# Kernel tuning notes

Measured on AMD Instinct MI355X. Metric: run time of the kernel, lower is better.

Reference implementation:

```python
import jax, jax.numpy as jnp
import numpy as np


def setup_inputs() -> dict:
    key = jax.random.key(0)
    k1, k2, k3 = jax.random.split(key, 3)
    B, N, C_IN, C_OUT = 8, 2048, 128, 64
    x = jax.random.normal(k1, (B, N, C_IN), dtype=jnp.float32)
    # Linear(c_in, c_out): weight [c_out, c_in], bias [c_out]
    W_adj = jax.random.normal(k2, (C_OUT, C_IN), dtype=jnp.float32) * (1.0 / np.sqrt(C_IN))
    b_adj = jax.random.normal(k3, (C_OUT,), dtype=jnp.float32) * 0.01
    return {"x": x, "W_adj": W_adj, "b_adj": b_adj}


def reference(x, W_adj, b_adj):
    # e_x = adj_projection(x): [B, N, C_out]
    e_x = jnp.einsum("bnc,oc->bno", x, W_adj) + b_adj
    # The original loop/concat builds all (i, j) pairs and takes per-pair
    # inner products; this is exactly the Gram matrix e_x @ e_x^T.
    lp = jax.nn.relu(jnp.tanh(jnp.einsum("bic,bjc->bij", e_x, e_x)))  # [B, N, N]
    num_neighbours = x.shape[1]
    node_feats = jnp.einsum("bij,bjc->bic", lp, e_x) / num_neighbours
    return node_feats, lp
```

## Files before the change

kernel.cpp:

```cpp
#include <hip/hip_runtime.h>
#include <hip/hip_bf16.h>


#define B_    8
#define N_    2048
#define D_    64
#define CIN_  128

typedef __bf16 bf16x8 __attribute__((ext_vector_type(8)));
typedef float f32x4  __attribute__((ext_vector_type(4)));

union FragU { uint4 u; bf16x8 f; };

static __device__ __forceinline__ bf16x8 ld_frag(const __hip_bfloat16* p) {
    FragU fu; fu.u = *reinterpret_cast<const uint4*>(p); return fu.f;
}

static __device__ __forceinline__ void st_frag(__hip_bfloat16* p, bf16x8 f) {
    FragU fu; fu.f = f; *reinterpret_cast<uint4*>(p) = fu.u;
}

static __device__ __forceinline__ void split8(const float* p, bf16x8& hi, bf16x8& lo) {
    const float4 a = *reinterpret_cast<const float4*>(p);
    const float4 b = *reinterpret_cast<const float4*>(p + 4);
    const float v[8] = {a.x, a.y, a.z, a.w, b.x, b.y, b.z, b.w};
#pragma unroll
    for (int i = 0; i < 8; i++) {
        const __bf16 h = (__bf16)v[i];
        hi[i] = h;
        lo[i] = (__bf16)(v[i] - (float)h);
    }
}

static __device__ __forceinline__ bf16x8 cvt8(const float* p) {
    const float4 a = *reinterpret_cast<const float4*>(p);
    const float4 b = *reinterpret_cast<const float4*>(p + 4);
    bf16x8 r;
    r[0] = (__bf16)a.x; r[1] = (__bf16)a.y; r[2] = (__bf16)a.z; r[3] = (__bf16)a.w;
    r[4] = (__bf16)b.x; r[5] = (__bf16)b.y; r[6] = (__bf16)b.z; r[7] = (__bf16)b.w;
    return r;
}

#define LDW  136

__global__ __launch_bounds__(256) void ex_kernel(
    const float* __restrict__ x,
    const float* __restrict__ W,
    const float* __restrict__ bias,
    __hip_bfloat16* __restrict__ e_hi,
    __hip_bfloat16* __restrict__ e_lo,
    __hip_bfloat16* __restrict__ e_hiT)
{
    __shared__ __align__(16) __hip_bfloat16 sW[2 * 64 * LDW];
    __hip_bfloat16* sWhi = sW;
    __hip_bfloat16* sWlo = sW + 64 * LDW;

    const int tid  = threadIdx.x;

#pragma unroll
    for (int p = 0; p < 4; p++) {
        const int q = tid + p * 256;
        const int r = q >> 4, c = (q & 15) * 8;
        bf16x8 hi, lo;
        split8(W + (size_t)r * CIN_ + c, hi, lo);
        st_frag(sWhi + r * LDW + c, hi);
        st_frag(sWlo + r * LDW + c, lo);
    }
    __syncthreads();

    const int w    = tid >> 6;
    const int lane = tid & 63;
    const int quad = lane >> 4;
    const int l16  = lane & 15;
    const int m0   = blockIdx.x * 64 + w * 16;

    const float* xrow = x + (size_t)(m0 + l16) * CIN_;
    bf16x8 ah[4], al[4];
#pragma unroll
    for (int ks = 0; ks < 4; ks++)
        split8(xrow + ks * 32 + quad * 8, ah[ks], al[ks]);

    f32x4 acc[4];
#pragma unroll
    for (int nt = 0; nt < 4; nt++) acc[nt] = f32x4{0.f, 0.f, 0.f, 0.f};

#pragma unroll
    for (int ks = 0; ks < 4; ks++) {
#pragma unroll
        for (int nt = 0; nt < 4; nt++) {
            bf16x8 wh = ld_frag(sWhi + (nt * 16 + l16) * LDW + ks * 32 + quad * 8);
            bf16x8 wl = ld_frag(sWlo + (nt * 16 + l16) * LDW + ks * 32 + quad * 8);
            acc[nt] = __builtin_amdgcn_mfma_f32_16x16x32_bf16(ah[ks], wh, acc[nt], 0, 0, 0);
            acc[nt] = __builtin_amdgcn_mfma_f32_16x16x32_bf16(ah[ks], wl, acc[nt], 0, 0, 0);
            acc[nt] = __builtin_amdgcn_mfma_f32_16x16x32_bf16(al[ks], wh, acc[nt], 0, 0, 0);
        }
    }

#pragma unroll
    for (int nt = 0; nt < 4; nt++) {
        const int chan = nt * 16 + l16;
        const float bv = bias[chan];
        union { __hip_bfloat16 h[4]; uint2 u2; } hv;
#pragma unroll
        for (int i = 0; i < 4; i++) {
            const int gr = m0 + quad * 4 + i;
            const float e = acc[nt][i] + bv;
            const __hip_bfloat16 hi = __float2bfloat16(e);
            const __hip_bfloat16 lo = __float2bfloat16(e - __bfloat162float(hi));
            e_hi[(size_t)gr * D_ + chan] = hi;
            e_lo[(size_t)gr * D_ + chan] = lo;
            hv.h[i] = hi;
        }
        const int gr0 = m0 + quad * 4;
        const int bt = gr0 >> 11, ir = gr0 & (N_ - 1);
        *reinterpret_cast<uint2*>(e_hiT + ((size_t)bt * D_ + chan) * N_ + ir) = hv.u2;
    }
}

#define LDE  72
#define LDT  136
#define LDF  132

__global__ __launch_bounds__(512, 4) void fused_kernel(
    const __hip_bfloat16* __restrict__ e_hi,
    const __hip_bfloat16* __restrict__ e_lo,
    const __hip_bfloat16* __restrict__ e_hiT,
    float* __restrict__ out)
{
    __shared__ __align__(16) unsigned char smem[32 * LDF * 4 + 128 * LDE * 2 * 2 + 64 * LDT * 2];
    float*          sLpF  = (float*)smem;
    __hip_bfloat16* sEhi  = (__hip_bfloat16*)(smem + 32 * LDF * 4);
    __hip_bfloat16* sElo  = sEhi + 128 * LDE;
    __hip_bfloat16* sEhiT = sElo + 128 * LDE;

    const int b   = blockIdx.x;
    const int i0  = blockIdx.y * 32;
    const int tid = threadIdx.x;
    const int w = tid >> 6, lane = tid & 63, quad = lane >> 4, l16 = lane & 15;
    const int g = w >> 2, h = w & 3;
    const int m0 = i0 + g * 16;

    const __hip_bfloat16* eih = e_hi + (size_t)(b * N_ + m0 + l16) * D_;
    const __hip_bfloat16* eil = e_lo + (size_t)(b * N_ + m0 + l16) * D_;
    bf16x8 ahi[2], alo[2];
#pragma unroll
    for (int ks = 0; ks < 2; ks++) {
        ahi[ks] = ld_frag(eih + ks * 32 + quad * 8);
        alo[ks] = ld_frag(eil + ks * 32 + quad * 8);
    }

    f32x4 o[4];
#pragma unroll
    for (int nt = 0; nt < 4; nt++) o[nt] = f32x4{0.f, 0.f, 0.f, 0.f};

    float* lp_out = out + (size_t)B_ * N_ * D_;

    for (int jt = 0; jt < 16; jt++) {
        const int j0 = jt * 128;
        __syncthreads();

#pragma unroll
        for (int p = 0; p < 2; p++) {
            const int q = tid + p * 512;
            {
                const int r = q >> 3, c = (q & 7) * 8;
                *(uint4*)(sEhi + r * LDE + c) =
                    *(const uint4*)(e_hi + (size_t)(b * N_ + j0 + r) * D_ + c);
                *(uint4*)(sElo + r * LDE + c) =
                    *(const uint4*)(e_lo + (size_t)(b * N_ + j0 + r) * D_ + c);
            }
            {
                const int r = q >> 4, c = (q & 15) * 8;
                *(uint4*)(sEhiT + r * LDT + c) =
                    *(const uint4*)(e_hiT + (size_t)(b * D_ + r) * N_ + j0 + c);
            }
        }
        __syncthreads();

#pragma unroll
        for (int nt = 0; nt < 2; nt++) {
            const int n0 = h * 32 + nt * 16;
            f32x4 s = f32x4{0.f, 0.f, 0.f, 0.f};
#pragma unroll
            for (int ks = 0; ks < 2; ks++) {
                const int koff = ks * 32 + quad * 8;
                bf16x8 bhi = ld_frag(sEhi + (n0 + l16) * LDE + koff);
                bf16x8 blo = ld_frag(sElo + (n0 + l16) * LDE + koff);
                s = __builtin_amdgcn_mfma_f32_16x16x32_bf16(ahi[ks], bhi, s, 0, 0, 0);
                s = __builtin_amdgcn_mfma_f32_16x16x32_bf16(ahi[ks], blo, s, 0, 0, 0);
                s = __builtin_amdgcn_mfma_f32_16x16x32_bf16(alo[ks], bhi, s, 0, 0, 0);
            }
#pragma unroll
            for (int i = 0; i < 4; i++) {
                const float tc = fmaxf(s[i], 0.0f);
                const float z = __builtin_amdgcn_exp2f(tc * -2.8853900817779268f);
                const float v = (1.0f - z) * __builtin_amdgcn_rcpf(1.0f + z);
                const int row = g * 16 + quad * 4 + i;
                const int col = n0 + l16;
                sLpF[row * LDF + col] = v;
            }
        }
        __syncthreads();

#pragma unroll
        for (int p = 0; p < 2; p++) {
            const int q = tid + p * 512;
            const int r = q >> 5, c = (q & 31) * 4;
            __builtin_nontemporal_store(
                *(const f32x4*)(sLpF + r * LDF + c),
                (f32x4*)(lp_out + ((size_t)(b * N_ + i0 + r)) * N_ + j0 + c));
        }

        {
            const int koff = h * 32 + quad * 8;
            bf16x8 a = cvt8(sLpF + (g * 16 + l16) * LDF + koff);
#pragma unroll
            for (int nt = 0; nt < 4; nt++) {
                bf16x8 bfr = ld_frag(sEhiT + (nt * 16 + l16) * LDT + koff);
                o[nt] = __builtin_amdgcn_mfma_f32_16x16x32_bf16(a, bfr, o[nt], 0, 0, 0);
            }
        }
    }

    __syncthreads();
    float* sO = (float*)smem;
#pragma unroll
    for (int nt = 0; nt < 4; nt++) {
#pragma unroll
        for (int i = 0; i < 4; i++) {
            const int row = quad * 4 + i;
            const int chan = nt * 16 + l16;
            sO[w * 1088 + row * 68 + chan] = o[nt][i];
        }
    }
    __syncthreads();
    {
        const int row = tid >> 4;
        const int c4  = (tid & 15) * 4;
        const int gg = row >> 4, rr = row & 15;
        const float* base = sO + (gg * 4) * 1088 + rr * 68 + c4;
        const float4 v0 = *(const float4*)(base);
        const float4 v1 = *(const float4*)(base + 1088);
        const float4 v2 = *(const float4*)(base + 2176);
        const float4 v3 = *(const float4*)(base + 3264);
        f32x4 r;
        r[0] = (v0.x + v1.x + v2.x + v3.x) * (1.0f / 2048.0f);
        r[1] = (v0.y + v1.y + v2.y + v3.y) * (1.0f / 2048.0f);
        r[2] = (v0.z + v1.z + v2.z + v3.z) * (1.0f / 2048.0f);
        r[3] = (v0.w + v1.w + v2.w + v3.w) * (1.0f / 2048.0f);
        __builtin_nontemporal_store(
            r, (f32x4*)(out + ((size_t)(b * N_ + i0 + row)) * D_ + c4));
    }
}

extern "C" void kernel_launch(void* const* d_in, const int* in_sizes, int n_in,
                              void* d_out, int out_size, void* d_ws, size_t ws_size,
                              hipStream_t stream) {
    const float* x    = (const float*)d_in[0];
    const float* W    = (const float*)d_in[1];
    const float* bias = (const float*)d_in[2];
    float* out = (float*)d_out;

    __hip_bfloat16* e_hi  = (__hip_bfloat16*)d_ws;
    __hip_bfloat16* e_lo  = e_hi + (size_t)B_ * N_ * D_;
    __hip_bfloat16* e_hiT = e_lo + (size_t)B_ * N_ * D_;

    ex_kernel<<<dim3(256), dim3(256), 0, stream>>>(x, W, bias, e_hi, e_lo, e_hiT);
    fused_kernel<<<dim3(8, 64), dim3(512), 0, stream>>>(e_hi, e_lo, e_hiT, out);
}
```

Before: 175.1 us.

## Load MFMA B-fragments directly from global memory instead of staging in LDS

Removes the per-tile cooperative staging of e_hi, e_lo and e_hiT into shared memory and has each wave read its MFMA operand fragments straight from global (L2/L1-cached) memory. This drops one barrier per tile and shrinks the LDS footprint to just the lp tile buffer, which could allow more resident blocks. In exchange, every wave issues redundant global loads of the same rows, relying on cache hits, and exposes that global latency directly before the MFMAs. The loop barrier is moved to the end of each iteration to protect reuse of the lp buffer.

```diff
diff --git a/kernel.cpp b/kernel.cpp
--- a/kernel.cpp
+++ b/kernel.cpp
@@ -117,8 +117,6 @@
     }
 }
 
-#define LDE  72
-#define LDT  136
 #define LDF  132
 
 __global__ __launch_bounds__(512, 4) void fused_kernel(
@@ -127,11 +125,8 @@
     const __hip_bfloat16* __restrict__ e_hiT,
     float* __restrict__ out)
 {
-    __shared__ __align__(16) unsigned char smem[32 * LDF * 4 + 128 * LDE * 2 * 2 + 64 * LDT * 2];
-    float*          sLpF  = (float*)smem;
-    __hip_bfloat16* sEhi  = (__hip_bfloat16*)(smem + 32 * LDF * 4);
-    __hip_bfloat16* sElo  = sEhi + 128 * LDE;
-    __hip_bfloat16* sEhiT = sElo + 128 * LDE;
+    __shared__ __align__(16) float smem[8 * 1088];
+    float* sLpF = smem;
 
     const int b   = blockIdx.x;
     const int i0  = blockIdx.y * 32;
@@ -157,35 +152,18 @@
 
     for (int jt = 0; jt < 16; jt++) {
         const int j0 = jt * 128;
-        __syncthreads();
-
-#pragma unroll
-        for (int p = 0; p < 2; p++) {
-            const int q = tid + p * 512;
-            {
-                const int r = q >> 3, c = (q & 7) * 8;
-                *(uint4*)(sEhi + r * LDE + c) =
-                    *(const uint4*)(e_hi + (size_t)(b * N_ + j0 + r) * D_ + c);
-                *(uint4*)(sElo + r * LDE + c) =
-                    *(const uint4*)(e_lo + (size_t)(b * N_ + j0 + r) * D_ + c);
-            }
-            {
-                const int r = q >> 4, c = (q & 15) * 8;
-                *(uint4*)(sEhiT + r * LDT + c) =
-                    *(const uint4*)(e_hiT + (size_t)(b * D_ + r) * N_ + j0 + c);
-            }
-        }
-        __syncthreads();
 
 #pragma unroll
         for (int nt = 0; nt < 2; nt++) {
             const int n0 = h * 32 + nt * 16;
+            const __hip_bfloat16* bjh = e_hi + (size_t)(b * N_ + j0 + n0 + l16) * D_;
+            const __hip_bfloat16* bjl = e_lo + (size_t)(b * N_ + j0 + n0 + l16) * D_;
             f32x4 s = f32x4{0.f, 0.f, 0.f, 0.f};
 #pragma unroll
             for (int ks = 0; ks < 2; ks++) {
                 const int koff = ks * 32 + quad * 8;
-                bf16x8 bhi = ld_frag(sEhi + (n0 + l16) * LDE + koff);
-                bf16x8 blo = ld_frag(sElo + (n0 + l16) * LDE + koff);
+                bf16x8 bhi = ld_frag(bjh + koff);
+                bf16x8 blo = ld_frag(bjl + koff);
                 s = __builtin_amdgcn_mfma_f32_16x16x32_bf16(ahi[ks], bhi, s, 0, 0, 0);
                 s = __builtin_amdgcn_mfma_f32_16x16x32_bf16(ahi[ks], blo, s, 0, 0, 0);
                 s = __builtin_amdgcn_mfma_f32_16x16x32_bf16(alo[ks], bhi, s, 0, 0, 0);
@@ -216,14 +194,15 @@
             bf16x8 a = cvt8(sLpF + (g * 16 + l16) * LDF + koff);
 #pragma unroll
             for (int nt = 0; nt < 4; nt++) {
-                bf16x8 bfr = ld_frag(sEhiT + (nt * 16 + l16) * LDT + koff);
+                bf16x8 bfr = ld_frag(
+                    e_hiT + ((size_t)(b * D_ + nt * 16 + l16)) * N_ + j0 + koff);
                 o[nt] = __builtin_amdgcn_mfma_f32_16x16x32_bf16(a, bfr, o[nt], 0, 0, 0);
             }
         }
-    }
-
-    __syncthreads();
-    float* sO = (float*)smem;
+        __syncthreads();
+    }
+
+    float* sO = smem;
 #pragma unroll
     for (int nt = 0; nt < 4; nt++) {
 #pragma unroll
```

Result: slower. 224.0 us (+27.9%).

## Prefetch next E tiles into registers and defer lp stores across barriers

Applied to the files above, without the earlier changes.

Loads the next j-tile of e_hi/e_lo/e_hiT into registers while the current tile is being computed, so global load latency overlaps MFMA work. The store of each lp tile is deferred until after the next iteration's barrier. The barrier between the tanh write and the second GEMM read is dropped, because each wave only reads the sLpF region it wrote itself. Barriers become a plain waitcnt plus s_barrier, and the final output store switches from nontemporal to a regular store. This raises register pressure and issues one wasted wrap-around prefetch on the last iteration.

```diff
diff --git a/kernel.cpp b/kernel.cpp
--- a/kernel.cpp
+++ b/kernel.cpp
@@ -39,6 +39,12 @@
     r[0] = (__bf16)a.x; r[1] = (__bf16)a.y; r[2] = (__bf16)a.z; r[3] = (__bf16)a.w;
     r[4] = (__bf16)b.x; r[5] = (__bf16)b.y; r[6] = (__bf16)b.z; r[7] = (__bf16)b.w;
     return r;
+}
+
+static __device__ __forceinline__ void lds_barrier() {
+    asm volatile("s_waitcnt lgkmcnt(0)" ::: "memory");
+    __builtin_amdgcn_s_barrier();
+    __builtin_amdgcn_sched_barrier(0);
 }
 
 #define LDW  136
@@ -139,6 +145,13 @@
     const int w = tid >> 6, lane = tid & 63, quad = lane >> 4, l16 = lane & 15;
     const int g = w >> 2, h = w & 3;
     const int m0 = i0 + g * 16;
+    const int koff = h * 32 + quad * 8;
+
+    const int q2 = tid + 512;
+    const int er1 = tid >> 3, ec1 = (tid & 7) * 8;
+    const int er2 = q2  >> 3, ec2 = (q2  & 7) * 8;
+    const int tr1 = tid >> 4, tc1 = (tid & 15) * 8;
+    const int tr2 = q2  >> 4, tc2 = (q2  & 15) * 8;
 
     const __hip_bfloat16* eih = e_hi + (size_t)(b * N_ + m0 + l16) * D_;
     const __hip_bfloat16* eil = e_lo + (size_t)(b * N_ + m0 + l16) * D_;
@@ -155,37 +168,59 @@
 
     float* lp_out = out + (size_t)B_ * N_ * D_;
 
+    uint4 gh0, gh1, gl0, gl1, gt0, gt1;
+    {
+        gh0 = *(const uint4*)(e_hi + (size_t)(b * N_ + er1) * D_ + ec1);
+        gh1 = *(const uint4*)(e_hi + (size_t)(b * N_ + er2) * D_ + ec2);
+        gl0 = *(const uint4*)(e_lo + (size_t)(b * N_ + er1) * D_ + ec1);
+        gl1 = *(const uint4*)(e_lo + (size_t)(b * N_ + er2) * D_ + ec2);
+        gt0 = *(const uint4*)(e_hiT + (size_t)(b * D_ + tr1) * N_ + tc1);
+        gt1 = *(const uint4*)(e_hiT + (size_t)(b * D_ + tr2) * N_ + tc2);
+    }
+
     for (int jt = 0; jt < 16; jt++) {
-        const int j0 = jt * 128;
-        __syncthreads();
-
-#pragma unroll
-        for (int p = 0; p < 2; p++) {
-            const int q = tid + p * 512;
-            {
-                const int r = q >> 3, c = (q & 7) * 8;
-                *(uint4*)(sEhi + r * LDE + c) =
-                    *(const uint4*)(e_hi + (size_t)(b * N_ + j0 + r) * D_ + c);
-                *(uint4*)(sElo + r * LDE + c) =
-                    *(const uint4*)(e_lo + (size_t)(b * N_ + j0 + r) * D_ + c);
+        lds_barrier();
+
+        if (jt > 0) {
+            const int jc0 = (jt - 1) * 128;
+#pragma unroll
+            for (int p = 0; p < 2; p++) {
+                const int q = tid + p * 512;
+                const int r = q >> 5, c = (q & 31) * 4;
+                __builtin_nontemporal_store(
+                    *(const f32x4*)(sLpF + r * LDF + c),
+                    (f32x4*)(lp_out + ((size_t)(b * N_ + i0 + r)) * N_ + jc0 + c));
             }
-            {
-                const int r = q >> 4, c = (q & 15) * 8;
-                *(uint4*)(sEhiT + r * LDT + c) =
-                    *(const uint4*)(e_hiT + (size_t)(b * D_ + r) * N_ + j0 + c);
-            }
-        }
-        __syncthreads();
-
-#pragma unroll
-        for (int nt = 0; nt < 2; nt++) {
-            const int n0 = h * 32 + nt * 16;
+        }
+
+        *(uint4*)(sEhi  + er1 * LDE + ec1) = gh0;
+        *(uint4*)(sEhi  + er2 * LDE + ec2) = gh1;
+        *(uint4*)(sElo  + er1 * LDE + ec1) = gl0;
+        *(uint4*)(sElo  + er2 * LDE + ec2) = gl1;
+        *(uint4*)(sEhiT + tr1 * LDT + tc1) = gt0;
+        *(uint4*)(sEhiT + tr2 * LDT + tc2) = gt1;
+
+        lds_barrier();
+
+        {
+            const int j0n = ((jt + 1) & 15) * 128;
+            gh0 = *(const uint4*)(e_hi + (size_t)(b * N_ + j0n + er1) * D_ + ec1);
+            gh1 = *(const uint4*)(e_hi + (size_t)(b * N_ + j0n + er2) * D_ + ec2);
+            gl0 = *(const uint4*)(e_lo + (size_t)(b * N_ + j0n + er1) * D_ + ec1);
+            gl1 = *(const uint4*)(e_lo + (size_t)(b * N_ + j0n + er2) * D_ + ec2);
+            gt0 = *(const uint4*)(e_hiT + (size_t)(b * D_ + tr1) * N_ + j0n + tc1);
+            gt1 = *(const uint4*)(e_hiT + (size_t)(b * D_ + tr2) * N_ + j0n + tc2);
+        }
+
+#pragma unroll
+        for (int ntl = 0; ntl < 2; ntl++) {
+            const int n0 = h * 32 + ntl * 16;
             f32x4 s = f32x4{0.f, 0.f, 0.f, 0.f};
 #pragma unroll
             for (int ks = 0; ks < 2; ks++) {
-                const int koff = ks * 32 + quad * 8;
-                bf16x8 bhi = ld_frag(sEhi + (n0 + l16) * LDE + koff);
-                bf16x8 blo = ld_frag(sElo + (n0 + l16) * LDE + koff);
+                const int ko = ks * 32 + quad * 8;
+                bf16x8 bhi = ld_frag(sEhi + (n0 + l16) * LDE + ko);
+                bf16x8 blo = ld_frag(sElo + (n0 + l16) * LDE + ko);
                 s = __builtin_amdgcn_mfma_f32_16x16x32_bf16(ahi[ks], bhi, s, 0, 0, 0);
                 s = __builtin_amdgcn_mfma_f32_16x16x32_bf16(ahi[ks], blo, s, 0, 0, 0);
                 s = __builtin_amdgcn_mfma_f32_16x16x32_bf16(alo[ks], bhi, s, 0, 0, 0);
@@ -195,34 +230,34 @@
                 const float tc = fmaxf(s[i], 0.0f);
                 const float z = __builtin_amdgcn_exp2f(tc * -2.8853900817779268f);
                 const float v = (1.0f - z) * __builtin_amdgcn_rcpf(1.0f + z);
-                const int row = g * 16 + quad * 4 + i;
-                const int col = n0 + l16;
-                sLpF[row * LDF + col] = v;
+                sLpF[(g * 16 + quad * 4 + i) * LDF + n0 + l16] = v;
             }
         }
-        __syncthreads();
-
+
+        {
+            bf16x8 a = cvt8(sLpF + (g * 16 + l16) * LDF + koff);
+#pragma unroll
+            for (int nt = 0; nt < 4; nt++) {
+                bf16x8 bfr = ld_frag(sEhiT + (nt * 16 + l16) * LDT + koff);
+                o[nt] = __builtin_amdgcn_mfma_f32_16x16x32_bf16(a, bfr, o[nt], 0, 0, 0);
+            }
+        }
+    }
+
+    lds_barrier();
+    {
+        const int jc0 = 15 * 128;
 #pragma unroll
         for (int p = 0; p < 2; p++) {
             const int q = tid + p * 512;
             const int r = q >> 5, c = (q & 31) * 4;
             __builtin_nontemporal_store(
                 *(const f32x4*)(sLpF + r * LDF + c),
-                (f32x4*)(lp_out + ((size_t)(b * N_ + i0 + r)) * N_ + j0 + c));
-        }
-
-        {
-            const int koff = h * 32 + quad * 8;
-            bf16x8 a = cvt8(sLpF + (g * 16 + l16) * LDF + koff);
-#pragma unroll
-            for (int nt = 0; nt < 4; nt++) {
-                bf16x8 bfr = ld_frag(sEhiT + (nt * 16 + l16) * LDT + koff);
-                o[nt] = __builtin_amdgcn_mfma_f32_16x16x32_bf16(a, bfr, o[nt], 0, 0, 0);
-            }
-        }
-    }
-
-    __syncthreads();
+                (f32x4*)(lp_out + ((size_t)(b * N_ + i0 + r)) * N_ + jc0 + c));
+        }
+    }
+    lds_barrier();
+
     float* sO = (float*)smem;
 #pragma unroll
     for (int nt = 0; nt < 4; nt++) {
@@ -233,7 +268,7 @@
             sO[w * 1088 + row * 68 + chan] = o[nt][i];
         }
     }
-    __syncthreads();
+    lds_barrier();
     {
         const int row = tid >> 4;
         const int c4  = (tid & 15) * 4;
@@ -248,8 +283,7 @@
         r[1] = (v0.y + v1.y + v2.y + v3.y) * (1.0f / 2048.0f);
         r[2] = (v0.z + v1.z + v2.z + v3.z) * (1.0f / 2048.0f);
         r[3] = (v0.w + v1.w + v2.w + v3.w) * (1.0f / 2048.0f);
-        __builtin_nontemporal_store(
-            r, (f32x4*)(out + ((size_t)(b * N_ + i0 + row)) * D_ + c4));
+        *reinterpret_cast<f32x4*>(out + ((size_t)(b * N_ + i0 + row)) * D_ + c4) = r;
     }
 }
 
```

Result: faster. 171.6 us (median of 2 runs) (-2.0%).
